# Kernel optimization log

Hardware: AMD Instinct MI355X
Metric: run time of the kernel (lower is better)

Reference implementation:

```python
import jax, jax.numpy as jnp
import numpy as np
from jax import lax

jax.config.update("jax_enable_x64", True)  # needed for the int64 fixed-point requant

B, H_IN, W_IN, CIN = 64, 226, 226, 32
KH, KW = 3, 3
H_OUT, W_OUT = H_IN - KH + 1, W_IN - KW + 1  # valid conv: 224x224


def setup_inputs() -> dict:
    key = jax.random.key(0)
    k1, k2, k3 = jax.random.split(key, 3)
    inp = jax.random.randint(k1, (B, H_IN, W_IN, CIN), -128, 128, dtype=jnp.int32)
    flt = jax.random.randint(k2, (B, KH, KW, CIN), -128, 128, dtype=jnp.int32)
    bias = jax.random.randint(k3, (B,), -1000, 1000, dtype=jnp.int32)
    return {
        "input": inp,
        "filt": flt,
        "bias": bias,
        "q_mantissa": 1518500250,  # ~0.7071 * 2^31, typical TFLite requant mantissa
        "exponent": -3,
        "output_zero_point": -5,
    }


def _multiply_by_quantize_mul(x_i64, q_mantissa: int, exponent: int):
    # Faithful to the source (note Python precedence: (q_mantissa + (1<<15)) >> 16)
    if q_mantissa < 2147418112:
        reduced_mantissa = (q_mantissa + (1 << 15)) >> 16
    else:
        reduced_mantissa = 32767
    total_shifts = 15 - exponent
    x = x_i64 * jnp.int64(reduced_mantissa)
    x = x + jnp.int64(1 << (total_shifts - 1))
    return x >> total_shifts  # arithmetic right shift, rounding-half-up


def reference(input, filt, bias, q_mantissa, exponent, output_zero_point):
    # Per-slice valid correlation with int32 accumulation:
    # acc[i,j,k] = sum_{m,n,o} input[i,j+m,k+n,o] * filt[i,m,n,o]
    def one_slice(x, w):
        # x: (H_IN, W_IN, CIN) int32, w: (KH, KW, CIN) int32 -> (H_OUT, W_OUT, 1)
        return lax.conv_general_dilated(
            x[None], w[..., None],  # NHWC, HWIO (Cout=1)
            window_strides=(1, 1), padding="VALID",
            dimension_numbers=("NHWC", "HWIO", "NHWC"),
            preferred_element_type=jnp.int32,
        )[0]

    acc = jax.vmap(one_slice)(input, filt)            # (B, H_OUT, W_OUT, 1) int32
    acc = acc + bias[:, None, None, None]             # int32 bias add
    acc = _multiply_by_quantize_mul(acc.astype(jnp.int64), int(q_mantissa), int(exponent))
    acc = acc + jnp.int64(output_zero_point)
    acc = jnp.clip(acc, -128, 127)
    return acc.astype(jnp.int8)                        # (B, H_OUT, W_OUT, 1)
```

## Files before the change

### kernel.cpp

```cpp
#include <hip/hip_runtime.h>


typedef int int4v __attribute__((ext_vector_type(4)));
typedef int int2v __attribute__((ext_vector_type(2)));

#define B_       64
#define H_IN_    226
#define W_IN_    226
#define CIN_     32
#define H_OUT_   224
#define W_OUT_   224
#define ROWP     (W_IN_ * CIN_)
#define IMGP     (H_IN_ * ROWP)
#define HB       28

__device__ __forceinline__ int pack4(int a, int b, int c, int d) {
    return (a & 0xff) | ((b & 0xff) << 8) | ((c & 0xff) << 16) | (d << 24);
}

__device__ __forceinline__ int dot4(int a, int b, int c) {
#if __has_builtin(__builtin_amdgcn_sdot4)
    return __builtin_amdgcn_sdot4(a, b, c, false);
#else
    return c + ((a << 24) >> 24) * ((b << 24) >> 24)
             + ((a << 16) >> 24) * ((b << 16) >> 24)
             + ((a << 8)  >> 24) * ((b << 8)  >> 24)
             + ( a        >> 24) * ( b        >> 24);
#endif
}

#define LOADRAW(row) {                                                  \
    const int* p_ = base + (row) * ROWP;                                \
    r[0] = *(const int4v*)(p_);                                         \
    r[1] = *(const int4v*)(p_ + CIN_);                                  \
    r[2] = *(const int4v*)(p_ + 2 * CIN_);                              \
    r[3] = *(const int4v*)(p_ + 3 * CIN_);                              \
}

#define PACK(slot) {                                                    \
    P[slot][0] = pack4(r[0][0], r[0][1], r[0][2], r[0][3]);             \
    P[slot][1] = pack4(r[1][0], r[1][1], r[1][2], r[1][3]);             \
    P[slot][2] = pack4(r[2][0], r[2][1], r[2][2], r[2][3]);             \
    P[slot][3] = pack4(r[3][0], r[3][1], r[3][2], r[3][3]);             \
}

#define BODY(s0, s1, s2, hh) {                                          \
    int a0 = 0, a1 = 0;                                                 \
    _Pragma("unroll")                                                   \
    for (int n = 0; n < 3; ++n) {                                       \
        a0 = dot4(P[s0][n],     F[0][n], a0);                           \
        a1 = dot4(P[s0][n + 1], F[0][n], a1);                           \
        a0 = dot4(P[s1][n],     F[1][n], a0);                           \
        a1 = dot4(P[s1][n + 1], F[1][n], a1);                           \
        a0 = dot4(P[s2][n],     F[2][n], a0);                           \
        a1 = dot4(P[s2][n + 1], F[2][n], a1);                           \
    }                                                                   \
    a0 += __shfl_xor(a0, 1); a0 += __shfl_xor(a0, 2); a0 += __shfl_xor(a0, 4); \
    a1 += __shfl_xor(a1, 1); a1 += __shfl_xor(a1, 2); a1 += __shfl_xor(a1, 4); \
    if (ci == 0) {                                                      \
        long long v0 = (((long long)(a0 + bi)) * rm + rnd) >> ts;       \
        long long v1 = (((long long)(a1 + bi)) * rm + rnd) >> ts;       \
        int i0 = (int)v0 + zp, i1 = (int)v1 + zp;                       \
        i0 = min(127, max(-128, i0));                                   \
        i1 = min(127, max(-128, i1));                                   \
        int2v o_; o_[0] = i0; o_[1] = i1;                               \
        *reinterpret_cast<int2v*>(ob + (hh) * W_OUT_) = o_;             \
    }                                                                   \
}

__global__ __launch_bounds__(256, 7) void conv2d_requant_kernel(
    const int* __restrict__ in,
    const int* __restrict__ filt,
    const int* __restrict__ bias,
    const int* __restrict__ qm_p,
    const int* __restrict__ ex_p,
    const int* __restrict__ zp_p,
    int* __restrict__ out)
{
    const int bx   = blockIdx.x;
    const int b    = bx / 28;
    const int seg  = bx % 28;
    const int widx = seg * 4 + (threadIdx.x >> 6);
    const int strip = widx / 14;
    const int wseg  = widx % 14;
    const int h0 = strip * HB;
    const int w0 = wseg * 16;
    const int lane = threadIdx.x & 63;
    const int wi = lane >> 3;
    const int ci = lane & 7;

    const int qm = qm_p[0];
    const int ex = ex_p[0];
    const int zp = zp_p[0];
    const int rm = (qm < 2147418112) ? ((qm + (1 << 15)) >> 16) : 32767;
    const int ts = 15 - ex;
    const long long rnd = 1LL << (ts - 1);
    const int bi = bias[b];

    int F[3][3];
    {
        const int* fb = filt + b * 288 + ci * 4;
#pragma unroll
        for (int m = 0; m < 3; ++m) {
#pragma unroll
            for (int n = 0; n < 3; ++n) {
                int4v t = *(const int4v*)(fb + (m * 3 + n) * CIN_);
                F[m][n] = pack4(t[0], t[1], t[2], t[3]);
            }
        }
    }

    const int* base = in + b * IMGP + h0 * ROWP + (w0 + 2 * wi) * CIN_ + ci * 4;
    int* ob = out + (b * H_OUT_ + h0) * W_OUT_ + w0 + 2 * wi;

    int P[3][4];
    int4v r[4];
    LOADRAW(0) PACK(0)
    LOADRAW(1) PACK(1)
    LOADRAW(2)

    for (int hh = 0; hh < 27; hh += 3) {
        PACK(2) LOADRAW(hh + 3) BODY(0, 1, 2, hh)
        PACK(0) LOADRAW(hh + 4) BODY(1, 2, 0, hh + 1)
        PACK(1) LOADRAW(hh + 5) BODY(2, 0, 1, hh + 2)
    }
    PACK(2) BODY(0, 1, 2, 27)
}

extern "C" void kernel_launch(void* const* d_in, const int* in_sizes, int n_in,
                              void* d_out, int out_size, void* d_ws, size_t ws_size,
                              hipStream_t stream) {
    const int* in   = (const int*)d_in[0];
    const int* filt = (const int*)d_in[1];
    const int* bias = (const int*)d_in[2];
    const int* qm   = (const int*)d_in[3];
    const int* ex   = (const int*)d_in[4];
    const int* zp   = (const int*)d_in[5];
    int* out = (int*)d_out;

    dim3 grid(B_ * 28);
    dim3 block(256);
    hipLaunchKernelGGL(conv2d_requant_kernel, grid, block, 0, stream,
                       in, filt, bias, qm, ex, zp, out);
}
```

Baseline: 104.0 us.

## Stage packed input rows in an LDS ring buffer with register-prefetched loads

Replaces the per-lane register sliding window with 1024-thread blocks, each covering a 56-row strip. Input rows are packed to int8x4 and kept in a 12-row LDS ring, and the next four rows are prefetched into registers while the current four output rows are computed. Each thread computes one output pixel over all 32 channels using 72 dot4 operations, so the cross-lane shuffle reduction goes away. The grid shrinks to 256 blocks at one block per CU with about 87KB of LDS, which risks poor latency hiding and LDS bank conflicts from the 32-byte-per-column stride.

```diff
diff --git a/kernel.cpp b/kernel.cpp
--- a/kernel.cpp
+++ b/kernel.cpp
@@ -2,17 +2,12 @@
 
 
 typedef int int4v __attribute__((ext_vector_type(4)));
-typedef int int2v __attribute__((ext_vector_type(2)));
 
-#define B_       64
-#define H_IN_    226
-#define W_IN_    226
-#define CIN_     32
-#define H_OUT_   224
-#define W_OUT_   224
-#define ROWP     (W_IN_ * CIN_)
-#define IMGP     (H_IN_ * ROWP)
-#define HB       28
+#define B_     64
+#define HB     56
+#define ROWU   1808
+#define NROWS  58
+#define RING   12
 
 __device__ __forceinline__ int pack4(int a, int b, int c, int d) {
     return (a & 0xff) | ((b & 0xff) << 8) | ((c & 0xff) << 16) | (d << 24);
@@ -29,65 +24,24 @@
 #endif
 }
 
-#define LOADRAW(row) {                                                  \
-    const int* p_ = base + (row) * ROWP;                                \
-    r[0] = *(const int4v*)(p_);                                         \
-    r[1] = *(const int4v*)(p_ + CIN_);                                  \
-    r[2] = *(const int4v*)(p_ + 2 * CIN_);                              \
-    r[3] = *(const int4v*)(p_ + 3 * CIN_);                              \
-}
-
-#define PACK(slot) {                                                    \
-    P[slot][0] = pack4(r[0][0], r[0][1], r[0][2], r[0][3]);             \
-    P[slot][1] = pack4(r[1][0], r[1][1], r[1][2], r[1][3]);             \
-    P[slot][2] = pack4(r[2][0], r[2][1], r[2][2], r[2][3]);             \
-    P[slot][3] = pack4(r[3][0], r[3][1], r[3][2], r[3][3]);             \
-}
-
-#define BODY(s0, s1, s2, hh) {                                          \
-    int a0 = 0, a1 = 0;                                                 \
-    _Pragma("unroll")                                                   \
-    for (int n = 0; n < 3; ++n) {                                       \
-        a0 = dot4(P[s0][n],     F[0][n], a0);                           \
-        a1 = dot4(P[s0][n + 1], F[0][n], a1);                           \
-        a0 = dot4(P[s1][n],     F[1][n], a0);                           \
-        a1 = dot4(P[s1][n + 1], F[1][n], a1);                           \
-        a0 = dot4(P[s2][n],     F[2][n], a0);                           \
-        a1 = dot4(P[s2][n + 1], F[2][n], a1);                           \
-    }                                                                   \
-    a0 += __shfl_xor(a0, 1); a0 += __shfl_xor(a0, 2); a0 += __shfl_xor(a0, 4); \
-    a1 += __shfl_xor(a1, 1); a1 += __shfl_xor(a1, 2); a1 += __shfl_xor(a1, 4); \
-    if (ci == 0) {                                                      \
-        long long v0 = (((long long)(a0 + bi)) * rm + rnd) >> ts;       \
-        long long v1 = (((long long)(a1 + bi)) * rm + rnd) >> ts;       \
-        int i0 = (int)v0 + zp, i1 = (int)v1 + zp;                       \
-        i0 = min(127, max(-128, i0));                                   \
-        i1 = min(127, max(-128, i1));                                   \
-        int2v o_; o_[0] = i0; o_[1] = i1;                               \
-        *reinterpret_cast<int2v*>(ob + (hh) * W_OUT_) = o_;             \
-    }                                                                   \
-}
-
-__global__ __launch_bounds__(256, 7) void conv2d_requant_kernel(
-    const int* __restrict__ in,
-    const int* __restrict__ filt,
-    const int* __restrict__ bias,
-    const int* __restrict__ qm_p,
-    const int* __restrict__ ex_p,
-    const int* __restrict__ zp_p,
+__global__ __launch_bounds__(1024, 1) void conv2d_requant_kernel(
+    const int4v* __restrict__ in4,
+    const int*  __restrict__ filt,
+    const int*  __restrict__ bias,
+    const int*  __restrict__ qm_p,
+    const int*  __restrict__ ex_p,
+    const int*  __restrict__ zp_p,
     int* __restrict__ out)
 {
-    const int bx   = blockIdx.x;
-    const int b    = bx / 28;
-    const int seg  = bx % 28;
-    const int widx = seg * 4 + (threadIdx.x >> 6);
-    const int strip = widx / 14;
-    const int wseg  = widx % 14;
-    const int h0 = strip * HB;
-    const int w0 = wseg * 16;
-    const int lane = threadIdx.x & 63;
-    const int wi = lane >> 3;
-    const int ci = lane & 7;
+    __shared__ int lds[RING][ROWU];
+
+    const int bx    = blockIdx.x;
+    const int b     = bx >> 2;
+    const int strip = bx & 3;
+    const int h0    = strip * HB;
+    const int t     = threadIdx.x;
+    const int col   = t & 255;
+    const int orow  = t >> 8;
 
     const int qm = qm_p[0];
     const int ex = ex_p[0];
@@ -97,40 +51,97 @@
     const long long rnd = 1LL << (ts - 1);
     const int bi = bias[b];
 
-    int F[3][3];
+    int fs[3][3][8];
     {
-        const int* fb = filt + b * 288 + ci * 4;
+        const int* fb = filt + b * 288;
 #pragma unroll
-        for (int m = 0; m < 3; ++m) {
+        for (int m = 0; m < 3; ++m)
 #pragma unroll
-            for (int n = 0; n < 3; ++n) {
-                int4v t = *(const int4v*)(fb + (m * 3 + n) * CIN_);
-                F[m][n] = pack4(t[0], t[1], t[2], t[3]);
+            for (int n = 0; n < 3; ++n)
+#pragma unroll
+                for (int c = 0; c < 8; ++c) {
+                    const int* p = fb + (m * 3 + n) * 32 + 4 * c;
+                    fs[m][n][c] = pack4(p[0], p[1], p[2], p[3]);
+                }
+    }
+
+    const int4v* gin = in4 + (b * 226 + h0) * ROWU;
+    const int outb = (b * 224 + h0) * 224;
+
+#pragma unroll
+    for (int r = 0; r < 6; ++r) {
+        int4v v = gin[r * ROWU + t];
+        lds[r][t] = pack4(v[0], v[1], v[2], v[3]);
+        if (t < ROWU - 1024) {
+            int4v w = gin[r * ROWU + t + 1024];
+            lds[r][t + 1024] = pack4(w[0], w[1], w[2], w[3]);
+        }
+    }
+    __syncthreads();
+
+    int curm = 0;
+    for (int s = 0; s < 14; ++s) {
+        const int cur = s * 4;
+
+        int4v g0[4], g1[4];
+#pragma unroll
+        for (int j = 0; j < 4; ++j) {
+            const int r = cur + 6 + j;
+            if (r < NROWS) {
+                g0[j] = gin[r * ROWU + t];
+                if (t < ROWU - 1024) g1[j] = gin[r * ROWU + t + 1024];
             }
         }
+
+        if (col < 224) {
+            int acc = 0;
+#pragma unroll
+            for (int m = 0; m < 3; ++m) {
+                int sl = curm + orow + m;
+                if (sl >= RING) sl -= RING;
+                const int* rp = &lds[sl][0];
+#pragma unroll
+                for (int n = 0; n < 3; ++n) {
+                    const int* cp = rp + (col + n) * 8;
+                    int4v lo = *(const int4v*)cp;
+                    int4v hi = *(const int4v*)(cp + 4);
+                    acc = dot4(lo[0], fs[m][n][0], acc);
+                    acc = dot4(lo[1], fs[m][n][1], acc);
+                    acc = dot4(lo[2], fs[m][n][2], acc);
+                    acc = dot4(lo[3], fs[m][n][3], acc);
+                    acc = dot4(hi[0], fs[m][n][4], acc);
+                    acc = dot4(hi[1], fs[m][n][5], acc);
+                    acc = dot4(hi[2], fs[m][n][6], acc);
+                    acc = dot4(hi[3], fs[m][n][7], acc);
+                }
+            }
+            long long v = (((long long)(acc + bi)) * rm + rnd) >> ts;
+            int q = (int)v + zp;
+            q = min(127, max(-128, q));
+            out[outb + (cur + orow) * 224 + col] = q;
+        }
+
+#pragma unroll
+        for (int j = 0; j < 4; ++j) {
+            const int r = cur + 6 + j;
+            if (r < NROWS) {
+                int sl = curm + 6 + j;
+                if (sl >= RING) sl -= RING;
+                lds[sl][t] = pack4(g0[j][0], g0[j][1], g0[j][2], g0[j][3]);
+                if (t < ROWU - 1024)
+                    lds[sl][t + 1024] = pack4(g1[j][0], g1[j][1], g1[j][2], g1[j][3]);
+            }
+        }
+        __syncthreads();
+        curm += 4;
+        if (curm >= RING) curm -= RING;
     }
-
-    const int* base = in + b * IMGP + h0 * ROWP + (w0 + 2 * wi) * CIN_ + ci * 4;
-    int* ob = out + (b * H_OUT_ + h0) * W_OUT_ + w0 + 2 * wi;
-
-    int P[3][4];
-    int4v r[4];
-    LOADRAW(0) PACK(0)
-    LOADRAW(1) PACK(1)
-    LOADRAW(2)
-
-    for (int hh = 0; hh < 27; hh += 3) {
-        PACK(2) LOADRAW(hh + 3) BODY(0, 1, 2, hh)
-        PACK(0) LOADRAW(hh + 4) BODY(1, 2, 0, hh + 1)
-        PACK(1) LOADRAW(hh + 5) BODY(2, 0, 1, hh + 2)
-    }
-    PACK(2) BODY(0, 1, 2, 27)
 }
 
 extern "C" void kernel_launch(void* const* d_in, const int* in_sizes, int n_in,
                               void* d_out, int out_size, void* d_ws, size_t ws_size,
                               hipStream_t stream) {
-    const int* in   = (const int*)d_in[0];
+    const int4v* in = (const int4v*)d_in[0];
     const int* filt = (const int*)d_in[1];
     const int* bias = (const int*)d_in[2];
     const int* qm   = (const int*)d_in[3];
@@ -138,8 +149,8 @@
     const int* zp   = (const int*)d_in[5];
     int* out = (int*)d_out;
 
-    dim3 grid(B_ * 28);
-    dim3 block(256);
+    dim3 grid(B_ * 4);
+    dim3 block(1024);
     hipLaunchKernelGGL(conv2d_requant_kernel, grid, block, 0, stream,
                        in, filt, bias, qm, ex, zp, out);
 }
```

New measurement: 102.5 us. About the same (-1.5%).
